# Kernel optimization log

Measured on AMD Instinct MI355X. Metric: run time of the kernel, lower is better.

The kernel has to match this reference:

```python
import jax, jax.numpy as jnp
import numpy as np

# LeNet-5 custom connectivity between S2 (6 ch) and C3 (16 ch): MAP[i, o] = 1 if input ch i feeds output ch o
MAP_INFO = np.array([
    [1, 0, 0, 0, 1, 1, 1, 0, 0, 1, 1, 1, 1, 0, 1, 1],
    [1, 1, 0, 0, 0, 1, 1, 1, 0, 0, 1, 1, 1, 1, 0, 1],
    [1, 1, 1, 0, 0, 0, 1, 1, 1, 0, 0, 1, 0, 1, 1, 1],
    [0, 1, 1, 1, 0, 0, 1, 1, 1, 1, 0, 0, 1, 0, 1, 1],
    [0, 0, 1, 1, 1, 0, 0, 1, 1, 1, 1, 0, 1, 1, 0, 1],
    [0, 0, 0, 1, 1, 1, 0, 0, 1, 1, 1, 1, 0, 1, 1, 1],
], dtype=np.float32)  # [6, 16]

SCALE = 1.7159
SLOPE = 2.0 / 3.0


def _conv(x, w):
    # x: [B, Cin, H, W], w: [Cout, Cin, kh, kw], VALID padding, stride 1
    return jax.lax.conv_general_dilated(
        x, w, window_strides=(1, 1), padding='VALID',
        dimension_numbers=('NCHW', 'OIHW', 'NCHW'))


def _subsample(x, w, b):
    # 2x2 average pool then per-channel affine (trainable scale/bias)
    B, C, H, W = x.shape
    p = x.reshape(B, C, H // 2, 2, W // 2, 2).mean(axis=(3, 5))
    return p * w[None, :, None, None] + b[None, :, None, None]


def _act(x):
    return SCALE * jnp.tanh(SLOPE * x)


def setup_inputs() -> dict:
    key = jax.random.key(0)
    ks = jax.random.split(key, 16)
    B = 8192

    def unif(k, shape, fan_in):
        return (jax.random.uniform(k, shape, dtype=jnp.float32) * 4.8 - 2.4) / fan_in

    x = jax.random.normal(ks[0], (B, 1, 32, 32), dtype=jnp.float32)
    c1_w = unif(ks[1], (6, 1, 5, 5), 25 * 1)
    c1_b = jax.random.uniform(ks[2], (6,), dtype=jnp.float32) * 0.1
    s2_w = unif(ks[3], (6,), 4)
    s2_b = jax.random.uniform(ks[4], (6,), dtype=jnp.float32)
    c3_w = unif(ks[5], (16, 6, 5, 5), 25 * 6)
    c3_b = jax.random.uniform(ks[6], (16,), dtype=jnp.float32) * 0.1
    s4_w = unif(ks[7], (16,), 4)
    s4_b = jax.random.uniform(ks[8], (16,), dtype=jnp.float32)
    c5_w = unif(ks[9], (120, 16, 5, 5), 25 * 16)
    c5_b = jax.random.uniform(ks[10], (120,), dtype=jnp.float32) * 0.1
    f6_w = unif(ks[11], (84, 120), 120)
    f6_b = jax.random.uniform(ks[12], (84,), dtype=jnp.float32) * 0.1
    rbf_w = jax.random.uniform(ks[13], (84, 10), dtype=jnp.float32)
    return dict(x=x, c1_w=c1_w, c1_b=c1_b, s2_w=s2_w, s2_b=s2_b,
                c3_w=c3_w, c3_b=c3_b, s4_w=s4_w, s4_b=s4_b,
                c5_w=c5_w, c5_b=c5_b, f6_w=f6_w, f6_b=f6_b, rbf_w=rbf_w)


def reference(x, c1_w, c1_b, s2_w, s2_b, c3_w, c3_b, s4_w, s4_b,
              c5_w, c5_b, f6_w, f6_b, rbf_w):
    # C1: 1->6 conv5, replicate padding 2 -> [B,6,32,32]
    xp = jnp.pad(x, ((0, 0), (0, 0), (2, 2), (2, 2)), mode='edge')
    h = _conv(xp, c1_w) + c1_b[None, :, None, None]
    # S2 + squashing act -> [B,6,16,16]
    h = _act(_subsample(h, s2_w, s2_b))
    # C3: sparse-connectivity conv expressed as dense conv with masked weights -> [B,16,12,12]
    mask = jnp.asarray(MAP_INFO.T)[:, :, None, None]  # [16,6,1,1]
    h = _conv(h, c3_w * mask) + c3_b[None, :, None, None]
    # S4 + act -> [B,16,6,6]
    h = _act(_subsample(h, s4_w, s4_b))
    # C5: 16->120 conv5 -> [B,120,1,1]
    h = _conv(h, c5_w) + c5_b[None, :, None, None]
    h = h.reshape(-1, 120)
    # F6 + act -> [B,84]
    h = _act(h @ f6_w.T + f6_b)
    # RBF output: squared euclidean distance to class prototypes -> [B,10]
    out = jnp.sum((h[:, :, None] - rbf_w[None, :, :]) ** 2, axis=1)
    return out
```

## Files before the change

kernel.cpp:

```cpp
#include <hip/hip_runtime.h>
#include <math.h>

typedef _Float16 h16;
typedef h16  h8v __attribute__((ext_vector_type(8)));
typedef h16  h4v __attribute__((ext_vector_type(4)));
typedef h16  h2v __attribute__((ext_vector_type(2)));
typedef float f4v __attribute__((ext_vector_type(4)));
typedef unsigned int u32;

#if defined(__has_builtin)
#if __has_builtin(__builtin_amdgcn_fdot2)
#define FDOT2(a,b,c) __builtin_amdgcn_fdot2((a),(b),(c),false)
#endif
#endif
#ifndef FDOT2
#define FDOT2(a,b,c) ((c) + (float)(a).x*(float)(b).x + (float)(a).y*(float)(b).y)
#endif

#define WS_K1H  0
#define WS_B1   216
#define WS_B3   224
#define WS_W3H  240
#define WS_W5H  2544
#define WS_F6H  35312
#define WS_RBFT 41456

#define L_B3    0
#define L_C5B   64
#define L_F6B   576
#define L_S2H   960
#define L_A5    960
#define L_HB    960
#define L_XPADH 14784
#define L_S4    20160
#define L_A6    20160
#define LDS_TOTAL 26304

__device__ const unsigned char MASK16[16] = {7,14,28,56,49,35,15,30,60,57,51,39,27,54,45,63};

__device__ __forceinline__ float squash(float x) {
    float z = (2.0f / 3.0f) * x;
    float a = fabsf(z);
    float e = __expf(-2.0f * a);
    float t = (1.0f - e) * __builtin_amdgcn_rcpf(1.0f + e);
    return copysignf(1.7159f * t, z);
}

__global__ __launch_bounds__(256) void prep_kernel(
    const float* __restrict__ c1_w, const float* __restrict__ c1_b,
    const float* __restrict__ s2_w, const float* __restrict__ s2_b,
    const float* __restrict__ c3_w, const float* __restrict__ c3_b,
    const float* __restrict__ s4_w, const float* __restrict__ s4_b,
    const float* __restrict__ c5_w, const float* __restrict__ f6_w,
    const float* __restrict__ rbf_w,
    float* __restrict__ ws)
{
    const int gid = blockIdx.x * 256 + threadIdx.x;
    const int gstr = gridDim.x * 256;
    h16* K1H = (h16*)ws;
    for (int idx = gid; idx < 216; idx += gstr) {
        int c = idx / 36, r = idx - c * 36;
        int u = r / 6, v = r - u * 6;
        float s = 0.f;
        #pragma unroll
        for (int dy = 0; dy < 2; ++dy)
            #pragma unroll
            for (int dx = 0; dx < 2; ++dx) {
                int ky = u - dy, kx = v - dx;
                if (ky >= 0 && ky < 5 && kx >= 0 && kx < 5)
                    s += c1_w[(c * 5 + ky) * 5 + kx];
            }
        K1H[idx] = (h16)(0.25f * s * s2_w[c]);
    }
    if (gid < 6)  ws[WS_B1 + gid] = s2_w[gid] * c1_b[gid] + s2_b[gid];
    if (gid < 16) ws[WS_B3 + gid] = s4_w[gid] * c3_b[gid] + s4_b[gid];
    h16* W3H = (h16*)(ws + WS_W3H);
    for (int idx = gid; idx < 4608; idx += gstr) {
        int i = idx / 768, r = idx - i * 768;
        int n = r / 48, k = r - n * 48;
        float val = 0.f;
        if (k < 36) {
            int u = k / 6, v = k - u * 6;
            float s = 0.f;
            #pragma unroll
            for (int dy = 0; dy < 2; ++dy)
                #pragma unroll
                for (int dx = 0; dx < 2; ++dx) {
                    int ky = u - dy, kx = v - dx;
                    if (ky >= 0 && ky < 5 && kx >= 0 && kx < 5)
                        s += c3_w[((n * 6 + i) * 5 + ky) * 5 + kx];
                }
            val = ((MASK16[n] >> i) & 1) ? 0.25f * s4_w[n] * s : 0.f;
        }
        W3H[idx] = (h16)val;
    }
    h16* W5H = (h16*)(ws + WS_W5H);
    for (int idx = gid; idx < 65536; idx += gstr) {
        int i = idx >> 12, r = idx & 4095;
        int n = r >> 5, k = r & 31;
        float val = (n < 120 && k < 25) ? c5_w[n * 400 + i * 25 + k] : 0.f;
        W5H[idx] = (h16)val;
    }
    h16* F6H = (h16*)(ws + WS_F6H);
    for (int idx = gid; idx < 12288; idx += gstr) {
        int n = idx >> 7, k = idx & 127;
        float val = (n < 84 && k < 120) ? f6_w[n * 120 + k] : 0.f;
        F6H[idx] = (h16)val;
    }
    for (int idx = gid; idx < 840; idx += gstr) {
        int k = idx / 10, c = idx - k * 10;
        ws[WS_RBFT + c * 84 + k] = rbf_w[idx];
    }
}

__global__ __launch_bounds__(256, 6) void lenet_kernel(
    const float* __restrict__ x,
    const float* __restrict__ c5_b, const float* __restrict__ f6_b,
    const float* __restrict__ ws,
    float* __restrict__ out)
{
    __shared__ __align__(16) char smem[LDS_TOTAL];
    float* s_b3  = (float*)(smem + L_B3);
    float* s_c5b = (float*)(smem + L_C5B);
    float* s_f6b = (float*)(smem + L_F6B);
    h16*  XPADH  = (h16*)(smem + L_XPADH);
    h16*  S2H    = (h16*)(smem + L_S2H);
    h16*  S4     = (h16*)(smem + L_S4);
    h16*  A5     = (h16*)(smem + L_A5);
    h16*  A6     = (h16*)(smem + L_A6);
    float* HB    = (float*)(smem + L_HB);

    const int tid  = threadIdx.x;
    const int wave = __builtin_amdgcn_readfirstlane(tid >> 6);
    const int lane = tid & 63;
    const int quad = lane >> 4;
    const int lr   = lane & 15;

    if (tid < 16)  s_b3[tid] = ws[WS_B3 + tid];
    if (tid < 128) s_c5b[tid] = (tid < 120) ? c5_b[tid] : 0.f;
    if (tid < 96)  s_f6b[tid] = (tid < 84) ? f6_b[tid] : 0.f;
    const float* xb = x + (size_t)blockIdx.x * 4096;
    for (int idx = tid; idx < 2880; idx += 256) {
        int img = idx / 720, r2 = idx - img * 720;
        int u = r2 / 20, v2 = r2 - u * 20;
        int sy = min(max(u - 2, 0), 31);
        int c0 = min(max(2 * v2 - 2, 0), 31);
        int c1 = min(max(2 * v2 - 1, 0), 31);
        const float* xr = xb + img * 1024 + sy * 32;
        h2v hv; hv.x = (h16)xr[c0]; hv.y = (h16)xr[c1];
        *(h2v*)(XPADH + img * 1440 + u * 40 + 2 * v2) = hv;
    }
    __syncthreads();

    {
        int py = tid >> 4, px = tid & 15;
        h2v win2[4][18];
        #pragma unroll
        for (int img = 0; img < 4; ++img) {
            const h16* basep = XPADH + img * 1440 + (2 * py) * 40 + 2 * px;
            #pragma unroll
            for (int u = 0; u < 6; ++u)
                #pragma unroll
                for (int p = 0; p < 3; ++p)
                    win2[img][u * 3 + p] = *(const h2v*)(basep + u * 40 + 2 * p);
        }
        const h2v* K1H = (const h2v*)ws;
        #pragma unroll
        for (int c = 0; c < 6; ++c) {
            float bias = ws[WS_B1 + c];
            h2v wv[18];
            #pragma unroll
            for (int j = 0; j < 18; ++j) wv[j] = K1H[c * 18 + j];
            #pragma unroll
            for (int img = 0; img < 4; ++img) {
                float acc = bias;
                #pragma unroll
                for (int j = 0; j < 18; ++j)
                    acc = FDOT2(win2[img][j], wv[j], acc);
                S2H[img * 1728 + c * 288 + py * 18 + px] = (h16)squash(acc);
            }
        }
    }
    __syncthreads();

    {
        const h16* W3H = (const h16*)(ws + WS_W3H);
        int o0, o1, o2, o3;
        {
            int k0 = 8 * quad;
            int u0 = k0 / 6, v0 = k0 - u0 * 6;  o0 = u0 * 18 + v0;
            int k1 = k0 + 2;
            int u1 = k1 / 6, v1 = k1 - u1 * 6;  o1 = u1 * 18 + v1;
            int k2 = k0 + 4;
            int u2 = k2 / 6, v2 = k2 - u2 * 6;  o2 = u2 * 18 + v2;
            int k3 = k0 + 6;
            int u3 = k3 / 6, v3 = k3 - u3 * 6;  o3 = u3 * 18 + v3;
        }
        int baseh0, baseh1, baseh2;
        {
            int m0 = wave * 16 + lr;
            int i0 = m0 / 36, p0 = m0 - i0 * 36;
            baseh0 = i0 * 1728 + (2 * (p0 / 6)) * 18 + 2 * (p0 % 6);
            int m1 = (wave + 4) * 16 + lr;
            int i1 = m1 / 36, p1 = m1 - i1 * 36;
            baseh1 = i1 * 1728 + (2 * (p1 / 6)) * 18 + 2 * (p1 % 6);
            int m2 = 128 + lr;
            int i2 = m2 / 36, p2 = m2 - i2 * 36;
            baseh2 = i2 * 1728 + (2 * (p2 / 6)) * 18 + 2 * (p2 % 6);
        }
        f4v cacc0 = {}, cacc1 = {}, cacc2 = {};
        const bool w0 = (wave == 0);
        #pragma unroll
        for (int i = 0; i < 6; ++i) {
            const h16* bbase = W3H + i * 768 + lr * 48;
            h8v w3a = *(const h8v*)(bbase + quad * 8);
            h4v w3b = *(const h4v*)(bbase + 32 + quad * 4);
            const h16* bp0 = S2H + baseh0 + i * 288;
            {
                union { u32 u[4]; h8v h; } av;
                av.u[0] = *(const u32*)(bp0 + o0);
                av.u[1] = *(const u32*)(bp0 + o1);
                av.u[2] = *(const u32*)(bp0 + o2);
                av.u[3] = *(const u32*)(bp0 + o3);
                cacc0 = __builtin_amdgcn_mfma_f32_16x16x32_f16(av.h, w3a, cacc0, 0, 0, 0);
                union { u32 u[2]; h4v h; } av2;
                av2.u[0] = *(const u32*)(bp0 + 92);
                av2.u[1] = *(const u32*)(bp0 + 94);
                cacc0 = __builtin_amdgcn_mfma_f32_16x16x16f16(av2.h, w3b, cacc0, 0, 0, 0);
            }
            const h16* bp1 = S2H + baseh1 + i * 288;
            {
                union { u32 u[4]; h8v h; } av;
                av.u[0] = *(const u32*)(bp1 + o0);
                av.u[1] = *(const u32*)(bp1 + o1);
                av.u[2] = *(const u32*)(bp1 + o2);
                av.u[3] = *(const u32*)(bp1 + o3);
                cacc1 = __builtin_amdgcn_mfma_f32_16x16x32_f16(av.h, w3a, cacc1, 0, 0, 0);
                union { u32 u[2]; h4v h; } av2;
                av2.u[0] = *(const u32*)(bp1 + 92);
                av2.u[1] = *(const u32*)(bp1 + 94);
                cacc1 = __builtin_amdgcn_mfma_f32_16x16x16f16(av2.h, w3b, cacc1, 0, 0, 0);
            }
            if (w0) {
                const h16* bp2 = S2H + baseh2 + i * 288;
                union { u32 u[4]; h8v h; } av;
                av.u[0] = *(const u32*)(bp2 + o0);
                av.u[1] = *(const u32*)(bp2 + o1);
                av.u[2] = *(const u32*)(bp2 + o2);
                av.u[3] = *(const u32*)(bp2 + o3);
                cacc2 = __builtin_amdgcn_mfma_f32_16x16x32_f16(av.h, w3a, cacc2, 0, 0, 0);
                union { u32 u[2]; h4v h; } av2;
                av2.u[0] = *(const u32*)(bp2 + 92);
                av2.u[1] = *(const u32*)(bp2 + 94);
                cacc2 = __builtin_amdgcn_mfma_f32_16x16x16f16(av2.h, w3b, cacc2, 0, 0, 0);
            }
        }
        float b3v = s_b3[lr];
        {
            #pragma unroll
            for (int r = 0; r < 4; ++r) {
                int m = wave * 16 + quad * 4 + r;
                int img = m / 36, pos = m - img * 36;
                S4[img * 672 + lr * 42 + pos] = (h16)squash(cacc0[r] + b3v);
            }
            #pragma unroll
            for (int r = 0; r < 4; ++r) {
                int m = (wave + 4) * 16 + quad * 4 + r;
                int img = m / 36, pos = m - img * 36;
                S4[img * 672 + lr * 42 + pos] = (h16)squash(cacc1[r] + b3v);
            }
            if (w0) {
                #pragma unroll
                for (int r = 0; r < 4; ++r) {
                    int m = 128 + quad * 4 + r;
                    int img = m / 36, pos = m - img * 36;
                    S4[img * 672 + lr * 42 + pos] = (h16)squash(cacc2[r] + b3v);
                }
            }
        }
    }
    __syncthreads();

    {
        {
            int m = tid >> 4, i = tid & 15;
            int img = m >> 2, q = m & 3, qy = q >> 1, qx = q & 1;
            const h16* s4b = S4 + img * 672 + i * 42 + qy * 6 + qx;
            h16* dst = A5 + m * 520 + i * 32;
            #pragma unroll
            for (int c = 0; c < 4; ++c) {
                h8v v;
                #pragma unroll
                for (int j = 0; j < 8; ++j) {
                    int k = c * 8 + j;
                    v[j] = (k < 25) ? s4b[(k / 5) * 6 + (k % 5)] : (h16)0.f;
                }
                *(h8v*)(dst + c * 8) = v;
            }
        }
        __syncthreads();
        const h16* W5H = (const h16*)(ws + WS_W5H);
        f4v dacc0 = {}, dacc1 = {};
        #pragma unroll
        for (int i = 0; i < 16; ++i) {
            h8v bf0 = *(const h8v*)(W5H + i * 4096 + (wave * 32 + lr) * 32 + quad * 8);
            h8v bf1 = *(const h8v*)(W5H + i * 4096 + (wave * 32 + 16 + lr) * 32 + quad * 8);
            h8v af0 = *(const h8v*)(A5 + lr * 520 + i * 32 + quad * 8);
            dacc0 = __builtin_amdgcn_mfma_f32_16x16x32_f16(af0, bf0, dacc0, 0, 0, 0);
            dacc1 = __builtin_amdgcn_mfma_f32_16x16x32_f16(af0, bf1, dacc1, 0, 0, 0);
        }
        if (tid < 64) {
            int m = tid >> 2, j = tid & 3;
            *(u32*)(A6 + m * 136 + 120 + 2 * j) = 0u;
        }
        {
            int n0 = wave * 32 + lr;
            if (n0 < 120) {
                int tt = n0 / 30, cb = (n0 - tt * 30) * 4;
                float bias = s_c5b[n0];
                #pragma unroll
                for (int r = 0; r < 4; ++r) {
                    int m = quad * 4 + r;
                    A6[((m >> 2) * 4 + tt) * 136 + cb + (m & 3)] = (h16)(dacc0[r] + bias);
                }
            }
            int n1 = wave * 32 + 16 + lr;
            if (n1 < 120) {
                int tt = n1 / 30, cb = (n1 - tt * 30) * 4;
                float bias = s_c5b[n1];
                #pragma unroll
                for (int r = 0; r < 4; ++r) {
                    int m = quad * 4 + r;
                    A6[((m >> 2) * 4 + tt) * 136 + cb + (m & 3)] = (h16)(dacc1[r] + bias);
                }
            }
        }
    }
    __syncthreads();

    {
        const h16* F6H = (const h16*)(ws + WS_F6H);
        f4v eacc0 = {}, eacc1 = {};
        const bool w2 = (wave < 2);
        #pragma unroll
        for (int kc = 0; kc < 4; ++kc) {
            h8v a8 = *(const h8v*)(A6 + lr * 136 + kc * 32 + quad * 8);
            h8v b0 = *(const h8v*)(F6H + (wave * 16 + lr) * 128 + kc * 32 + quad * 8);
            eacc0 = __builtin_amdgcn_mfma_f32_16x16x32_f16(a8, b0, eacc0, 0, 0, 0);
            if (w2) {
                h8v b1 = *(const h8v*)(F6H + ((wave + 4) * 16 + lr) * 128 + kc * 32 + quad * 8);
                eacc1 = __builtin_amdgcn_mfma_f32_16x16x32_f16(a8, b1, eacc1, 0, 0, 0);
            }
        }
        {
            int n = wave * 16 + lr;
            float bias = s_f6b[n];
            #pragma unroll
            for (int r = 0; r < 4; ++r) {
                int m = quad * 4 + r;
                HB[m * 88 + n] = squash(eacc0[r] + bias);
            }
        }
        if (w2) {
            int n = (wave + 4) * 16 + lr;
            if (n < 84) {
                float bias = s_f6b[n];
                #pragma unroll
                for (int r = 0; r < 4; ++r) {
                    int m = quad * 4 + r;
                    HB[m * 88 + n] = squash(eacc1[r] + bias);
                }
            }
        }
    }
    __syncthreads();

    if (tid < 160) {
        int m = tid / 10, cls = tid - m * 10;
        const float4* hr = (const float4*)(HB + m * 88);
        const float4* pr = (const float4*)(ws + WS_RBFT + cls * 84);
        float a = 0.f;
        #pragma unroll
        for (int u = 0; u < 21; ++u) {
            float4 hv = hr[u], pv = pr[u];
            float dx = hv.x - pv.x, dy = hv.y - pv.y;
            float dz = hv.z - pv.z, dw = hv.w - pv.w;
            a += dx * dx + dy * dy + dz * dz + dw * dw;
        }
        out[(size_t)blockIdx.x * 160 + tid] = a;
    }
}

extern "C" void kernel_launch(void* const* d_in, const int* in_sizes, int n_in,
                              void* d_out, int out_size, void* d_ws, size_t ws_size,
                              hipStream_t stream) {
    (void)n_in; (void)out_size; (void)ws_size;
    const float* x     = (const float*)d_in[0];
    const float* c1_w  = (const float*)d_in[1];
    const float* c1_b  = (const float*)d_in[2];
    const float* s2_w  = (const float*)d_in[3];
    const float* s2_b  = (const float*)d_in[4];
    const float* c3_w  = (const float*)d_in[5];
    const float* c3_b  = (const float*)d_in[6];
    const float* s4_w  = (const float*)d_in[7];
    const float* s4_b  = (const float*)d_in[8];
    const float* c5_w  = (const float*)d_in[9];
    const float* c5_b  = (const float*)d_in[10];
    const float* f6_w  = (const float*)d_in[11];
    const float* f6_b  = (const float*)d_in[12];
    const float* rbf_w = (const float*)d_in[13];
    float* out = (float*)d_out;
    float* ws  = (float*)d_ws;

    const int B = in_sizes[0] / 1024;

    prep_kernel<<<256, 256, 0, stream>>>(c1_w, c1_b, s2_w, s2_b, c3_w, c3_b,
                                         s4_w, s4_b, c5_w, f6_w, rbf_w, ws);
    lenet_kernel<<<B / 4, 256, 0, stream>>>(x, c5_b, f6_b, ws, out);
}
```

Before: 143.8 us.

## Drop padded-input LDS staging and alias LDS buffers to raise occupancy

The C1 stage now builds its 6x6 input windows straight from global memory with clamped float2 loads, so the padded half-precision input tile in LDS and one barrier go away. The LDS regions are re-aliased: S4 moves up, A6 and HB overlap the A5/S2H region, and extra barriers are added so the overlapping buffers are not overwritten while still in use. Total LDS per block shrinks and launch bounds rise from 6 to 8 blocks per CU, aiming for more resident waves. In exchange, each input element is reloaded from global or cache by several threads, the loads are less coalesced, and register pressure may limit the higher occupancy.

Measured after the change: 150.2 us. 1.04x slower.

```diff
diff --git a/kernel.cpp b/kernel.cpp
--- a/kernel.cpp
+++ b/kernel.cpp
@@ -30,11 +30,10 @@
 #define L_F6B   576
 #define L_S2H   960
 #define L_A5    960
-#define L_HB    960
-#define L_XPADH 14784
-#define L_S4    20160
-#define L_A6    20160
-#define LDS_TOTAL 26304
+#define L_A6    960
+#define L_HB    6592
+#define L_S4    14784
+#define LDS_TOTAL 20160
 
 __device__ const unsigned char MASK16[16] = {7,14,28,56,49,35,15,30,60,57,51,39,27,54,45,63};
 
@@ -113,7 +112,7 @@
     }
 }
 
-__global__ __launch_bounds__(256, 6) void lenet_kernel(
+__global__ __launch_bounds__(256, 8) void lenet_kernel(
     const float* __restrict__ x,
     const float* __restrict__ c5_b, const float* __restrict__ f6_b,
     const float* __restrict__ ws,
@@ -123,7 +122,6 @@
     float* s_b3  = (float*)(smem + L_B3);
     float* s_c5b = (float*)(smem + L_C5B);
     float* s_f6b = (float*)(smem + L_F6B);
-    h16*  XPADH  = (h16*)(smem + L_XPADH);
     h16*  S2H    = (h16*)(smem + L_S2H);
     h16*  S4     = (h16*)(smem + L_S4);
     h16*  A5     = (h16*)(smem + L_A5);
@@ -139,44 +137,38 @@
     if (tid < 16)  s_b3[tid] = ws[WS_B3 + tid];
     if (tid < 128) s_c5b[tid] = (tid < 120) ? c5_b[tid] : 0.f;
     if (tid < 96)  s_f6b[tid] = (tid < 84) ? f6_b[tid] : 0.f;
-    const float* xb = x + (size_t)blockIdx.x * 4096;
-    for (int idx = tid; idx < 2880; idx += 256) {
-        int img = idx / 720, r2 = idx - img * 720;
-        int u = r2 / 20, v2 = r2 - u * 20;
-        int sy = min(max(u - 2, 0), 31);
-        int c0 = min(max(2 * v2 - 2, 0), 31);
-        int c1 = min(max(2 * v2 - 1, 0), 31);
-        const float* xr = xb + img * 1024 + sy * 32;
-        h2v hv; hv.x = (h16)xr[c0]; hv.y = (h16)xr[c1];
-        *(h2v*)(XPADH + img * 1440 + u * 40 + 2 * v2) = hv;
-    }
-    __syncthreads();
 
     {
+        const float* xb = x + (size_t)blockIdx.x * 4096;
         int py = tid >> 4, px = tid & 15;
-        h2v win2[4][18];
+        const bool pxlo = (px == 0), pxhi = (px == 15);
+        int cb0 = pxlo ? 0 : (2 * px - 2);
+        int cb1 = 2 * px;
+        int cb2 = pxhi ? 30 : (2 * px + 2);
+        const h2v* K1H = (const h2v*)ws;
         #pragma unroll
         for (int img = 0; img < 4; ++img) {
-            const h16* basep = XPADH + img * 1440 + (2 * py) * 40 + 2 * px;
-            #pragma unroll
-            for (int u = 0; u < 6; ++u)
-                #pragma unroll
-                for (int p = 0; p < 3; ++p)
-                    win2[img][u * 3 + p] = *(const h2v*)(basep + u * 40 + 2 * p);
-        }
-        const h2v* K1H = (const h2v*)ws;
-        #pragma unroll
-        for (int c = 0; c < 6; ++c) {
-            float bias = ws[WS_B1 + c];
-            h2v wv[18];
-            #pragma unroll
-            for (int j = 0; j < 18; ++j) wv[j] = K1H[c * 18 + j];
-            #pragma unroll
-            for (int img = 0; img < 4; ++img) {
-                float acc = bias;
+            const float* xi = xb + img * 1024;
+            h2v win2[18];
+            #pragma unroll
+            for (int u = 0; u < 6; ++u) {
+                int ry = min(max(2 * py - 2 + u, 0), 31);
+                const float* xr = xi + ry * 32;
+                float2 p0 = *(const float2*)(xr + cb0);
+                float2 p1 = *(const float2*)(xr + cb1);
+                float2 p2 = *(const float2*)(xr + cb2);
+                if (pxlo) p0.y = p0.x;
+                if (pxhi) p2.x = p2.y;
+                win2[u * 3 + 0] = h2v{(h16)p0.x, (h16)p0.y};
+                win2[u * 3 + 1] = h2v{(h16)p1.x, (h16)p1.y};
+                win2[u * 3 + 2] = h2v{(h16)p2.x, (h16)p2.y};
+            }
+            #pragma unroll
+            for (int c = 0; c < 6; ++c) {
+                float acc = ws[WS_B1 + c];
                 #pragma unroll
                 for (int j = 0; j < 18; ++j)
-                    acc = FDOT2(win2[img][j], wv[j], acc);
+                    acc = FDOT2(win2[j], K1H[c * 18 + j], acc);
                 S2H[img * 1728 + c * 288 + py * 18 + px] = (h16)squash(acc);
             }
         }
@@ -256,44 +248,51 @@
             }
         }
         float b3v = s_b3[lr];
-        {
+        #pragma unroll
+        for (int r = 0; r < 4; ++r) {
+            int m = wave * 16 + quad * 4 + r;
+            int img = m / 36, pos = m - img * 36;
+            S4[img * 672 + lr * 42 + pos] = (h16)squash(cacc0[r] + b3v);
+        }
+        #pragma unroll
+        for (int r = 0; r < 4; ++r) {
+            int m = (wave + 4) * 16 + quad * 4 + r;
+            int img = m / 36, pos = m - img * 36;
+            S4[img * 672 + lr * 42 + pos] = (h16)squash(cacc1[r] + b3v);
+        }
+        if (w0) {
             #pragma unroll
             for (int r = 0; r < 4; ++r) {
-                int m = wave * 16 + quad * 4 + r;
+                int m = 128 + quad * 4 + r;
                 int img = m / 36, pos = m - img * 36;
-                S4[img * 672 + lr * 42 + pos] = (h16)squash(cacc0[r] + b3v);
-            }
-            #pragma unroll
-            for (int r = 0; r < 4; ++r) {
-                int m = (wave + 4) * 16 + quad * 4 + r;
-                int img = m / 36, pos = m - img * 36;
-                S4[img * 672 + lr * 42 + pos] = (h16)squash(cacc1[r] + b3v);
-            }
-            if (w0) {
-                #pragma unroll
-                for (int r = 0; r < 4; ++r) {
-                    int m = 128 + quad * 4 + r;
-                    int img = m / 36, pos = m - img * 36;
-                    S4[img * 672 + lr * 42 + pos] = (h16)squash(cacc2[r] + b3v);
-                }
+                S4[img * 672 + lr * 42 + pos] = (h16)squash(cacc2[r] + b3v);
             }
         }
     }
     __syncthreads();
 
     {
-        {
-            int m = tid >> 4, i = tid & 15;
-            int img = m >> 2, q = m & 3, qy = q >> 1, qx = q & 1;
-            const h16* s4b = S4 + img * 672 + i * 42 + qy * 6 + qx;
-            h16* dst = A5 + m * 520 + i * 32;
+        const int mD = tid >> 4, iD = tid & 15;
+        h16 sreg[25];
+        {
+            int img = mD >> 2, q = mD & 3, qy = q >> 1, qx = q & 1;
+            const h16* s4b = S4 + img * 672 + iD * 42 + qy * 6 + qx;
+            #pragma unroll
+            for (int r = 0; r < 5; ++r)
+                #pragma unroll
+                for (int c = 0; c < 5; ++c)
+                    sreg[r * 5 + c] = s4b[r * 6 + c];
+        }
+        __syncthreads();
+        {
+            h16* dst = A5 + mD * 520 + iD * 32;
             #pragma unroll
             for (int c = 0; c < 4; ++c) {
                 h8v v;
                 #pragma unroll
                 for (int j = 0; j < 8; ++j) {
                     int k = c * 8 + j;
-                    v[j] = (k < 25) ? s4b[(k / 5) * 6 + (k % 5)] : (h16)0.f;
+                    v[j] = (k < 25) ? sreg[k] : (h16)0.f;
                 }
                 *(h8v*)(dst + c * 8) = v;
             }
@@ -309,6 +308,7 @@
             dacc0 = __builtin_amdgcn_mfma_f32_16x16x32_f16(af0, bf0, dacc0, 0, 0, 0);
             dacc1 = __builtin_amdgcn_mfma_f32_16x16x32_f16(af0, bf1, dacc1, 0, 0, 0);
         }
+        __syncthreads();
         if (tid < 64) {
             int m = tid >> 2, j = tid & 3;
             *(u32*)(A6 + m * 136 + 120 + 2 * j) = 0u;
```
